# Kernel tuning notes

Hardware: AMD Instinct MI355X
Metric: run time of the kernel (lower is better)

## Reference

```python
import jax, jax.numpy as jnp
import numpy as np

N_NODES = 50000
N_EDGES = 800000
N_GRAPHS = 8
BN_EPS = 1e-5


def setup_inputs() -> dict:
    key = jax.random.key(0)
    ks = iter(jax.random.split(key, 40))
    d = {}
    d["x"] = jax.random.normal(next(ks), (N_NODES, 3), dtype=jnp.float32)
    d["edge_index"] = jax.random.randint(next(ks), (2, N_EDGES), 0, N_NODES, dtype=jnp.int32)
    d["batch"] = jnp.sort(jax.random.randint(next(ks), (N_NODES,), 0, N_GRAPHS, dtype=jnp.int32))
    conv_in = [3, 64, 128]  # dense concat widths feeding each GCN layer
    for i, cin in enumerate(conv_in):
        d[f"W{i}"] = jax.random.normal(next(ks), (cin, 64), dtype=jnp.float32) * (1.0 / np.sqrt(cin))
        d[f"b{i}"] = jax.random.normal(next(ks), (64,), dtype=jnp.float32) * 0.05
        d[f"g{i}"] = jax.random.uniform(next(ks), (64,), dtype=jnp.float32) + 0.5
        d[f"beta{i}"] = jax.random.normal(next(ks), (64,), dtype=jnp.float32) * 0.05
        d[f"rm{i}"] = jax.random.normal(next(ks), (64,), dtype=jnp.float32) * 0.05
        d[f"rv{i}"] = jax.random.uniform(next(ks), (64,), dtype=jnp.float32) + 0.5
    def lin(k, i, o):
        return (jax.random.normal(k, (i, o), dtype=jnp.float32) * (1.0 / np.sqrt(i)),)
    d["enc_w0"], = lin(next(ks), 256, 128); d["enc_b0"] = jax.random.normal(next(ks), (128,), jnp.float32) * 0.05
    d["enc_w1"], = lin(next(ks), 128, 64); d["enc_b1"] = jax.random.normal(next(ks), (64,), jnp.float32) * 0.05
    d["dec_w0"], = lin(next(ks), 64, 32); d["dec_b0"] = jax.random.normal(next(ks), (32,), jnp.float32) * 0.05
    d["dec_w1"], = lin(next(ks), 32, 1); d["dec_b1"] = jax.random.normal(next(ks), (1,), jnp.float32) * 0.05
    return d


def reference(x, edge_index, batch,
              W0, b0, g0, beta0, rm0, rv0,
              W1, b1, g1, beta1, rm1, rv1,
              W2, b2, g2, beta2, rm2, rv2,
              enc_w0, enc_b0, enc_w1, enc_b1,
              dec_w0, dec_b0, dec_w1, dec_b1):
    N = x.shape[0]
    loops = jnp.arange(N, dtype=edge_index.dtype)
    src = jnp.concatenate([edge_index[0], loops])  # GCNConv adds self loops
    dst = jnp.concatenate([edge_index[1], loops])
    deg = jax.ops.segment_sum(jnp.ones_like(src, dtype=x.dtype), dst, num_segments=N)
    dinv = jnp.where(deg > 0, jax.lax.rsqrt(deg), 0.0)
    coef = (dinv[src] * dinv[dst])[:, None]  # symmetric normalization per edge

    def conv_bn_relu(h, W, b, g, beta, rm, rv):
        hw = h @ W                                    # [N, 64]
        out = jax.ops.segment_sum(hw[src] * coef, dst, num_segments=N) + b
        out = (out - rm) * (g * jax.lax.rsqrt(rv + BN_EPS)) + beta  # BN eval mode
        return jax.nn.relu(out)

    params = [(W0, b0, g0, beta0, rm0, rv0),
              (W1, b1, g1, beta1, rm1, rv1),
              (W2, b2, g2, beta2, rm2, rv2)]
    prev = []
    h = x
    for p in params:  # dense connectivity: concat all previous concat-outputs
        h = conv_bn_relu(h, *p)
        h = jnp.concatenate(prev + [h], axis=1)
        prev.append(h)

    e = jax.nn.relu(jax.nn.relu(h @ enc_w0 + enc_b0) @ enc_w1 + enc_b1)  # [N, 64]
    counts = jax.ops.segment_sum(jnp.ones((N,), x.dtype), batch, num_segments=N_GRAPHS)
    gfeat = jax.ops.segment_sum(e, batch, num_segments=N_GRAPHS) / jnp.maximum(counts, 1.0)[:, None]
    out = jax.nn.relu(gfeat @ dec_w0 + dec_b0) @ dec_w1 + dec_b1  # [G, 1]
    return out[:, 0]  # torch.squeeze(output, 1) since num_classes == 1
```

## Files before the change

kernel.cpp:

```cpp
#include <hip/hip_runtime.h>
#include <hip/hip_fp16.h>

#define NN 50000
#define NE 800000
#define NG 8
#define BN_EPS 1e-5f
#define NBLK ((NN + 255) / 256)
#define POOL_BLOCKS 512
#define NPART 8
#define HLD 192

typedef __attribute__((ext_vector_type(8))) short bf16x8;
typedef __attribute__((ext_vector_type(4))) float f32x4;

static __device__ __forceinline__ unsigned short f2bf(float f) {
    unsigned int u = __float_as_uint(f);
    unsigned int r = (u + 0x7FFFu + ((u >> 16) & 1u)) >> 16;
    return (unsigned short)r;
}
static __device__ __forceinline__ float bf2f(unsigned short h) {
    return __uint_as_float((unsigned int)h << 16);
}


__global__ __launch_bounds__(256) void count_deg(const int* __restrict__ dst,
                                                 int* __restrict__ degi) {
    int e = blockIdx.x * 256 + threadIdx.x;
    if (e < NE) atomicAdd(&degi[dst[e]], 1);
}

__global__ __launch_bounds__(256) void compute_dinv_xs(const int* __restrict__ degi,
                                                       const float* __restrict__ x,
                                                       float* __restrict__ dinv,
                                                       float* __restrict__ xs) {
    int i = blockIdx.x * 256 + threadIdx.x;
    if (i < NN) {
        float di = rsqrtf((float)(degi[i] + 1));
        dinv[i] = di;
        xs[i * 3 + 0] = x[i * 3 + 0] * di;
        xs[i * 3 + 1] = x[i * 3 + 1] * di;
        xs[i * 3 + 2] = x[i * 3 + 2] * di;
    }
}

__global__ __launch_bounds__(256) void scan_partial(const int* __restrict__ degi,
                                                    int* __restrict__ rowptr,
                                                    int* __restrict__ bsum) {
    __shared__ int sh[256];
    const int tid = threadIdx.x;
    const int i = blockIdx.x * 256 + tid;
    int v = (i < NN) ? degi[i] : 0;
    sh[tid] = v;
    __syncthreads();
#pragma unroll
    for (int off = 1; off < 256; off <<= 1) {
        int t = (tid >= off) ? sh[tid - off] : 0;
        __syncthreads();
        sh[tid] += t;
        __syncthreads();
    }
    if (i < NN) rowptr[i] = sh[tid] - v;
    if (tid == 255) bsum[blockIdx.x] = sh[255];
}

__global__ __launch_bounds__(256) void scan_bsums(int* __restrict__ bsum) {
    __shared__ int sh[256];
    const int tid = threadIdx.x;
    int v = (tid < NBLK) ? bsum[tid] : 0;
    sh[tid] = v;
    __syncthreads();
#pragma unroll
    for (int off = 1; off < 256; off <<= 1) {
        int t = (tid >= off) ? sh[tid - off] : 0;
        __syncthreads();
        sh[tid] += t;
        __syncthreads();
    }
    if (tid < NBLK) bsum[tid] = sh[tid] - v;
}

__global__ __launch_bounds__(256) void scan_finalize(const int* __restrict__ bsum,
                                                     int* __restrict__ rowptr,
                                                     int* __restrict__ cursor) {
    const int i = blockIdx.x * 256 + threadIdx.x;
    if (i < NN) {
        int r = rowptr[i] + bsum[blockIdx.x];
        rowptr[i] = r;
        cursor[i] = r;
    }
    if (i == 0) rowptr[NN] = NE;
}

__global__ __launch_bounds__(256) void fill_csr(const int* __restrict__ src,
                                                const int* __restrict__ dst,
                                                int* __restrict__ cursor,
                                                unsigned short* __restrict__ esrc16) {
    int e = blockIdx.x * 256 + threadIdx.x;
    if (e < NE) {
        int s = src[e], d = dst[e];
        int p = atomicAdd(&cursor[d], 1);
        esrc16[p] = (unsigned short)s;
    }
}


__global__ __launch_bounds__(256) void pack_w(const float* __restrict__ W, int K, int NOUT,
                                              unsigned short* __restrict__ ph,
                                              unsigned short* __restrict__ pl) {
    int idx = blockIdx.x * 256 + threadIdx.x;
    if (idx >= K * NOUT) return;
    int j = idx & 7;
    int lane = (idx >> 3) & 63;
    int rest = idx >> 9;
    int NF = NOUT >> 4;
    int f = rest % NF, ks = rest / NF;
    int k = ks * 32 + (lane >> 4) * 8 + j;
    int col = f * 16 + (lane & 15);
    float v = W[k * NOUT + col];
    unsigned short hi = f2bf(v);
    ph[idx] = hi;
    pl[idx] = f2bf(v - bf2f(hi));
}

__global__ __launch_bounds__(256) void pack_we0(const float* __restrict__ W,
                                                unsigned short* __restrict__ ph,
                                                unsigned short* __restrict__ pl) {
    const int K = 192, NOUT = 128;
    int idx = blockIdx.x * 256 + threadIdx.x;
    if (idx >= K * NOUT) return;
    int j = idx & 7;
    int lane = (idx >> 3) & 63;
    int rest = idx >> 9;
    int NF = NOUT >> 4;
    int f = rest % NF, ks = rest / NF;
    int k = ks * 32 + (lane >> 4) * 8 + j;
    int col = f * 16 + (lane & 15);
    float v = (k < 64) ? (W[k * NOUT + col] + W[(k + 64) * NOUT + col])
                       : W[(k + 64) * NOUT + col];
    unsigned short hi = f2bf(v);
    ph[idx] = hi;
    pl[idx] = f2bf(v - bf2f(hi));
}


template<int K, int NF, int MODE>
__global__ __launch_bounds__(256) void mfma_gemm(
        const unsigned short* __restrict__ Ahi,
        const unsigned short* __restrict__ Alo, int lda,
        const unsigned short* __restrict__ Bph,
        const unsigned short* __restrict__ Bpl,
        const float* __restrict__ bias,
        const float* __restrict__ dinv,
        float* __restrict__ outF,
        __half* __restrict__ outH,
        unsigned short* __restrict__ outHi,
        unsigned short* __restrict__ outLo, int ldo) {
    const int wave = threadIdx.x >> 6;
    const int lane = threadIdx.x & 63;
    const int rbase = blockIdx.x * 64 + wave * 16;
    int arow = rbase + (lane & 15);
    if (arow >= NN) arow = NN - 1;
    const int kbase = (lane >> 4) * 8;

    f32x4 acc[NF];
#pragma unroll
    for (int f = 0; f < NF; f++) acc[f] = (f32x4){0.f, 0.f, 0.f, 0.f};

    const unsigned short* pa_hi = Ahi + (size_t)arow * lda + kbase;
    const unsigned short* pa_lo = Alo + (size_t)arow * lda + kbase;
    const unsigned short* pb_hi = Bph + lane * 8;
    const unsigned short* pb_lo = Bpl + lane * 8;

#pragma unroll
    for (int ks = 0; ks < K / 32; ks++) {
        bf16x8 ah = *reinterpret_cast<const bf16x8*>(pa_hi + ks * 32);
        bf16x8 al = *reinterpret_cast<const bf16x8*>(pa_lo + ks * 32);
#pragma unroll
        for (int f = 0; f < NF; f++) {
            bf16x8 bh = *reinterpret_cast<const bf16x8*>(pb_hi + (size_t)((ks * NF + f) * 64) * 8);
            bf16x8 bl = *reinterpret_cast<const bf16x8*>(pb_lo + (size_t)((ks * NF + f) * 64) * 8);
            acc[f] = __builtin_amdgcn_mfma_f32_16x16x32_bf16(ah, bh, acc[f], 0, 0, 0);
            acc[f] = __builtin_amdgcn_mfma_f32_16x16x32_bf16(ah, bl, acc[f], 0, 0, 0);
            acc[f] = __builtin_amdgcn_mfma_f32_16x16x32_bf16(al, bh, acc[f], 0, 0, 0);
        }
    }

    const int drow0 = rbase + (lane >> 4) * 4;
    const int dcol = lane & 15;
#pragma unroll
    for (int f = 0; f < NF; f++) {
#pragma unroll
        for (int r = 0; r < 4; r++) {
            int row = drow0 + r;
            if (row < NN) {
                int col = f * 16 + dcol;
                float v = acc[f][r];
                if (MODE == 0) {
                    outH[(size_t)row * 64 + col] = __float2half(v * dinv[row]);
                } else {
                    v = fmaxf(v + bias[col], 0.0f);
                    if (MODE == 1) {
                        unsigned short hi = f2bf(v);
                        outHi[(size_t)row * ldo + col] = hi;
                        outLo[(size_t)row * ldo + col] = f2bf(v - bf2f(hi));
                    } else {
                        outF[(size_t)row * ldo + col] = v;
                    }
                }
            }
        }
    }
}


__global__ __launch_bounds__(256) void agg_x3(
        const float* __restrict__ xs,
        const int* __restrict__ rowptr,
        const unsigned short* __restrict__ esrc16,
        const float* __restrict__ dinv,
        float* __restrict__ ax) {
    const int i = blockIdx.x * 256 + threadIdx.x;
    if (i >= NN) return;
    float a0 = xs[i * 3 + 0];
    float a1 = xs[i * 3 + 1];
    float a2 = xs[i * 3 + 2];
    const int beg = rowptr[i], end = rowptr[i + 1];
    int e = beg;
    for (; e + 3 < end; e += 4) {
        int s0 = esrc16[e], s1 = esrc16[e + 1], s2 = esrc16[e + 2], s3 = esrc16[e + 3];
        a0 += xs[s0 * 3 + 0] + xs[s1 * 3 + 0] + xs[s2 * 3 + 0] + xs[s3 * 3 + 0];
        a1 += xs[s0 * 3 + 1] + xs[s1 * 3 + 1] + xs[s2 * 3 + 1] + xs[s3 * 3 + 1];
        a2 += xs[s0 * 3 + 2] + xs[s1 * 3 + 2] + xs[s2 * 3 + 2] + xs[s3 * 3 + 2];
    }
    for (; e < end; e++) {
        int s = esrc16[e];
        a0 += xs[s * 3 + 0];
        a1 += xs[s * 3 + 1];
        a2 += xs[s * 3 + 2];
    }
    const float di = dinv[i];
    ax[i * 3 + 0] = a0 * di;
    ax[i * 3 + 1] = a1 * di;
    ax[i * 3 + 2] = a2 * di;
}


__global__ __launch_bounds__(256) void l0_bn_relu(
        const float* __restrict__ ax, const float* __restrict__ W0,
        const float* __restrict__ b, const float* __restrict__ g,
        const float* __restrict__ beta, const float* __restrict__ rm,
        const float* __restrict__ rv,
        unsigned short* __restrict__ Hhi, unsigned short* __restrict__ Hlo) {
    const int t = blockIdx.x * 256 + threadIdx.x;
    const int row = t >> 6;
    const int ch = t & 63;
    if (row >= NN) return;
    float a0 = ax[row * 3 + 0], a1 = ax[row * 3 + 1], a2 = ax[row * 3 + 2];
    float v = a0 * W0[0 * 64 + ch] + a1 * W0[1 * 64 + ch] + a2 * W0[2 * 64 + ch] + b[ch];
    float sc = g[ch] * rsqrtf(rv[ch] + BN_EPS);
    v = (v - rm[ch]) * sc + beta[ch];
    v = fmaxf(v, 0.0f);
    unsigned short hi = f2bf(v);
    Hhi[(size_t)row * HLD + ch] = hi;
    Hlo[(size_t)row * HLD + ch] = f2bf(v - bf2f(hi));
}


__global__ __launch_bounds__(256) void gather_bn_relu(
        const __half2* __restrict__ tab2,
        const int* __restrict__ rowptr,
        const unsigned short* __restrict__ esrc16,
        const float* __restrict__ dinv,
        const float* __restrict__ b, const float* __restrict__ g,
        const float* __restrict__ beta, const float* __restrict__ rm,
        const float* __restrict__ rv,
        unsigned short* __restrict__ Hhi, unsigned short* __restrict__ Hlo, int cbase) {
    const int wid = (blockIdx.x * 256 + threadIdx.x) >> 6;
    const int lane = threadIdx.x & 63;
    const int c2 = lane & 31;
    const int grp = lane >> 5;
    if (wid >= NN) return;
    const int beg = rowptr[wid], end = rowptr[wid + 1];
    float a0 = 0.0f, a1 = 0.0f;
    int e = beg + grp;
    for (; e + 6 < end; e += 8) {
        int s0 = esrc16[e], s1 = esrc16[e + 2], s2 = esrc16[e + 4], s3 = esrc16[e + 6];
        float2 f0 = __half22float2(tab2[(size_t)s0 * 32 + c2]);
        float2 f1 = __half22float2(tab2[(size_t)s1 * 32 + c2]);
        float2 f2 = __half22float2(tab2[(size_t)s2 * 32 + c2]);
        float2 f3 = __half22float2(tab2[(size_t)s3 * 32 + c2]);
        a0 += (f0.x + f1.x) + (f2.x + f3.x);
        a1 += (f0.y + f1.y) + (f2.y + f3.y);
    }
    for (; e < end; e += 2) {
        float2 f = __half22float2(tab2[(size_t)esrc16[e] * 32 + c2]);
        a0 += f.x;
        a1 += f.y;
    }
    a0 += __shfl_xor(a0, 32, 64);
    a1 += __shfl_xor(a1, 32, 64);
    float2 fs = __half22float2(tab2[(size_t)wid * 32 + c2]);
    a0 += fs.x;
    a1 += fs.y;
    const float di = dinv[wid];
    a0 *= di;
    a1 *= di;
    const int ch0 = 2 * c2, ch1 = 2 * c2 + 1;
    float v0 = (a0 + b[ch0] - rm[ch0]) * (g[ch0] * rsqrtf(rv[ch0] + BN_EPS)) + beta[ch0];
    float v1 = (a1 + b[ch1] - rm[ch1]) * (g[ch1] * rsqrtf(rv[ch1] + BN_EPS)) + beta[ch1];
    v0 = fmaxf(v0, 0.0f);
    v1 = fmaxf(v1, 0.0f);
    if (grp == 0) {
        unsigned short h0 = f2bf(v0), h1 = f2bf(v1);
        unsigned short l0 = f2bf(v0 - bf2f(h0)), l1 = f2bf(v1 - bf2f(h1));
        size_t o = (size_t)wid * HLD + cbase + ch0;
        *reinterpret_cast<unsigned int*>(&Hhi[o]) = (unsigned int)h0 | ((unsigned int)h1 << 16);
        *reinterpret_cast<unsigned int*>(&Hlo[o]) = (unsigned int)l0 | ((unsigned int)l1 << 16);
    }
}


__global__ __launch_bounds__(256) void pool_kernel(
        const float* __restrict__ e, const int* __restrict__ batch,
        float* __restrict__ gfeat_part, float* __restrict__ counts_part) {
    __shared__ float sh[4][NG][64];
    __shared__ float shc[4][NG];
    const int tid = threadIdx.x;
    const int ch = tid & 63;
    const int rg = tid >> 6;
    float acc[NG];
    float cnt[NG];
#pragma unroll
    for (int g = 0; g < NG; g++) { acc[g] = 0.0f; cnt[g] = 0.0f; }
    for (int i = blockIdx.x * 4 + rg; i < NN; i += POOL_BLOCKS * 4) {
        int b = batch[i];
        float v = e[i * 64 + ch];
#pragma unroll
        for (int g = 0; g < NG; g++) {
            acc[g] += (b == g) ? v : 0.0f;
            cnt[g] += (b == g) ? 1.0f : 0.0f;
        }
    }
#pragma unroll
    for (int g = 0; g < NG; g++) sh[rg][g][ch] = acc[g];
    if (ch == 0) {
#pragma unroll
        for (int g = 0; g < NG; g++) shc[rg][g] = cnt[g];
    }
    __syncthreads();
    const int p = blockIdx.x & (NPART - 1);
    if (rg == 0) {
#pragma unroll
        for (int g = 0; g < NG; g++) {
            float s = sh[0][g][ch] + sh[1][g][ch] + sh[2][g][ch] + sh[3][g][ch];
            atomicAdd(&gfeat_part[(p * NG + g) * 64 + ch], s);
        }
    }
    if (tid < NG) {
        float s = shc[0][tid] + shc[1][tid] + shc[2][tid] + shc[3][tid];
        atomicAdd(&counts_part[p * NG + tid], s);
    }
}


__global__ __launch_bounds__(256) void dec_kernel(
        const float* __restrict__ gfeat_part, const float* __restrict__ counts_part,
        const float* __restrict__ w0, const float* __restrict__ b0,
        const float* __restrict__ w1, const float* __restrict__ b1,
        float* __restrict__ out) {
    __shared__ float mg[NG][64];
    __shared__ float mc[NG];
    __shared__ float t1[NG][32];
    const int tid = threadIdx.x;
    for (int idx = tid; idx < NG * 64; idx += 256) {
        float s = 0.0f;
#pragma unroll
        for (int p = 0; p < NPART; p++) s += gfeat_part[p * NG * 64 + idx];
        mg[idx >> 6][idx & 63] = s;
    }
    if (tid < NG) {
        float s = 0.0f;
#pragma unroll
        for (int p = 0; p < NPART; p++) s += counts_part[p * NG + tid];
        mc[tid] = s;
    }
    __syncthreads();
    const int g = tid >> 5, c = tid & 31;
    float inv = 1.0f / fmaxf(mc[g], 1.0f);
    float acc = b0[c];
    for (int k = 0; k < 64; k++)
        acc = fmaf(mg[g][k] * inv, w0[k * 32 + c], acc);
    t1[g][c] = fmaxf(acc, 0.0f);
    __syncthreads();
    if (tid < NG) {
        float o = b1[0];
        for (int c2 = 0; c2 < 32; c2++) o = fmaf(t1[tid][c2], w1[c2], o);
        out[tid] = o;
    }
}


extern "C" void kernel_launch(void* const* d_in, const int* in_sizes, int n_in,
                              void* d_out, int out_size, void* d_ws, size_t ws_size,
                              hipStream_t stream) {
    const float* x      = (const float*)d_in[0];
    const int*   ei     = (const int*)d_in[1];
    const int*   batch  = (const int*)d_in[2];
    const float* W0     = (const float*)d_in[3];
    const float* b0     = (const float*)d_in[4];
    const float* g0     = (const float*)d_in[5];
    const float* beta0  = (const float*)d_in[6];
    const float* rm0    = (const float*)d_in[7];
    const float* rv0    = (const float*)d_in[8];
    const float* W1     = (const float*)d_in[9];
    const float* b1     = (const float*)d_in[10];
    const float* g1     = (const float*)d_in[11];
    const float* beta1  = (const float*)d_in[12];
    const float* rm1    = (const float*)d_in[13];
    const float* rv1    = (const float*)d_in[14];
    const float* W2     = (const float*)d_in[15];
    const float* b2     = (const float*)d_in[16];
    const float* g2     = (const float*)d_in[17];
    const float* beta2  = (const float*)d_in[18];
    const float* rm2    = (const float*)d_in[19];
    const float* rv2    = (const float*)d_in[20];
    const float* enc_w0 = (const float*)d_in[21];
    const float* enc_b0 = (const float*)d_in[22];
    const float* enc_w1 = (const float*)d_in[23];
    const float* enc_b1 = (const float*)d_in[24];
    const float* dec_w0 = (const float*)d_in[25];
    const float* dec_b0 = (const float*)d_in[26];
    const float* dec_w1 = (const float*)d_in[27];
    const float* dec_b1 = (const float*)d_in[28];

    const int* esrc = ei;
    const int* edst = ei + NE;

    char* wsb = (char*)d_ws;
    unsigned short* Hhi = (unsigned short*)wsb;
    unsigned short* Hlo = Hhi + (size_t)NN * HLD;
    char* U = (char*)(Hlo + (size_t)NN * HLD);
    unsigned short* Thi = (unsigned short*)U;
    unsigned short* Tlo = Thi + (size_t)NN * 128;
    int*   degi   = (int*)U;
    int*   rowptr = degi + NN;
    int*   cursor = rowptr + NN + 1;
    unsigned short* esrc16 = (unsigned short*)(cursor + NN);
    float* hws    = (float*)(U + (size_t)NN * 128 * 2 * sizeof(unsigned short));
    __half* tabh  = (__half*)hws;
    float* dinv   = hws + (size_t)NN * 64;
    float* xs     = dinv + NN;
    float* ax     = xs + (size_t)NN * 3;
    float* gfeat_part  = ax + (size_t)NN * 3;
    float* counts_part = gfeat_part + NPART * NG * 64;
    int*   bsum   = (int*)(counts_part + NPART * NG);
    unsigned short* wp = (unsigned short*)(bsum + NBLK);
    unsigned short* Wp1h = wp;              unsigned short* Wp1l = Wp1h + 64 * 64;
    unsigned short* Wp2h = Wp1l + 64 * 64;  unsigned short* Wp2l = Wp2h + 128 * 64;
    unsigned short* We0h = Wp2l + 128 * 64; unsigned short* We0l = We0h + 192 * 128;
    unsigned short* We1h = We0l + 192 * 128;unsigned short* We1l = We1h + 128 * 64;

    hipMemsetAsync(gfeat_part, 0, (NPART * NG * 64 + NPART * NG) * sizeof(float), stream);
    hipMemsetAsync(degi, 0, NN * sizeof(int), stream);

    count_deg<<<(NE + 255) / 256, 256, 0, stream>>>(edst, degi);
    compute_dinv_xs<<<NBLK, 256, 0, stream>>>(degi, x, dinv, xs);
    scan_partial<<<NBLK, 256, 0, stream>>>(degi, rowptr, bsum);
    scan_bsums<<<1, 256, 0, stream>>>(bsum);
    scan_finalize<<<NBLK, 256, 0, stream>>>(bsum, rowptr, cursor);
    fill_csr<<<(NE + 255) / 256, 256, 0, stream>>>(esrc, edst, cursor, esrc16);

    pack_w<<<(64 * 64 + 255) / 256, 256, 0, stream>>>(W1, 64, 64, Wp1h, Wp1l);
    pack_w<<<(128 * 64 + 255) / 256, 256, 0, stream>>>(W2, 128, 64, Wp2h, Wp2l);
    pack_we0<<<(192 * 128 + 255) / 256, 256, 0, stream>>>(enc_w0, We0h, We0l);
    pack_w<<<(128 * 64 + 255) / 256, 256, 0, stream>>>(enc_w1, 128, 64, We1h, We1l);

    const int GRID_MFMA = (NN + 63) / 64;
    const int GRID_64   = (NN * 64 + 255) / 256;

    agg_x3<<<NBLK, 256, 0, stream>>>(xs, rowptr, esrc16, dinv, ax);
    l0_bn_relu<<<GRID_64, 256, 0, stream>>>(ax, W0, b0, g0, beta0, rm0, rv0, Hhi, Hlo);

    mfma_gemm<64, 4, 0><<<GRID_MFMA, 256, 0, stream>>>(Hhi, Hlo, HLD, Wp1h, Wp1l,
                                                       nullptr, dinv, nullptr, tabh, nullptr, nullptr, 0);
    gather_bn_relu<<<GRID_64, 256, 0, stream>>>((const __half2*)tabh, rowptr, esrc16, dinv,
                                                b1, g1, beta1, rm1, rv1, Hhi, Hlo, 64);

    mfma_gemm<128, 4, 0><<<GRID_MFMA, 256, 0, stream>>>(Hhi, Hlo, HLD, Wp2h, Wp2l,
                                                        nullptr, dinv, nullptr, tabh, nullptr, nullptr, 0);
    gather_bn_relu<<<GRID_64, 256, 0, stream>>>((const __half2*)tabh, rowptr, esrc16, dinv,
                                                b2, g2, beta2, rm2, rv2, Hhi, Hlo, 128);

    mfma_gemm<192, 8, 1><<<GRID_MFMA, 256, 0, stream>>>(Hhi, Hlo, HLD, We0h, We0l,
                                                        enc_b0, nullptr, nullptr, nullptr, Thi, Tlo, 128);
    mfma_gemm<128, 4, 2><<<GRID_MFMA, 256, 0, stream>>>(Thi, Tlo, 128, We1h, We1l,
                                                        enc_b1, nullptr, hws, nullptr, nullptr, nullptr, 64);

    pool_kernel<<<POOL_BLOCKS, 256, 0, stream>>>(hws, batch, gfeat_part, counts_part);
    dec_kernel<<<1, 256, 0, stream>>>(gfeat_part, counts_part, dec_w0, dec_b0, dec_w1, dec_b1, (float*)d_out);
}
```

Baseline: 260.5 us.

## Fuse encoder GEMMs with mean pooling and merge small setup kernels

Fuses the two encoder GEMMs and the graph pooling into one kernel. The first GEMM's output stays in LDS and is re-split into bf16 hi/lo pairs for the second GEMM, and results are pooled through shared-memory atomics. This removes the global round trips for the 128-wide intermediate and the 64-wide encoder output, plus the separate pool kernel. The dinv/xs computation is folded into the scan kernel, the four weight-packing launches become one, and per-graph counts come from a binary search over the sorted batch array. The cost is more shared-memory atomics, LDS pressure from a 34KB buffer, and one extra block-wide sync.

```diff
diff --git a/kernel.cpp b/kernel.cpp
--- a/kernel.cpp
+++ b/kernel.cpp
@@ -6,7 +6,6 @@
 #define NG 8
 #define BN_EPS 1e-5f
 #define NBLK ((NN + 255) / 256)
-#define POOL_BLOCKS 512
 #define NPART 8
 #define HLD 192
 
@@ -29,27 +28,23 @@
     if (e < NE) atomicAdd(&degi[dst[e]], 1);
 }
 
-__global__ __launch_bounds__(256) void compute_dinv_xs(const int* __restrict__ degi,
-                                                       const float* __restrict__ x,
-                                                       float* __restrict__ dinv,
-                                                       float* __restrict__ xs) {
-    int i = blockIdx.x * 256 + threadIdx.x;
+__global__ __launch_bounds__(256) void scan_partial(const int* __restrict__ degi,
+                                                    const float* __restrict__ x,
+                                                    int* __restrict__ rowptr,
+                                                    int* __restrict__ bsum,
+                                                    float* __restrict__ dinv,
+                                                    float* __restrict__ xs) {
+    __shared__ int sh[256];
+    const int tid = threadIdx.x;
+    const int i = blockIdx.x * 256 + tid;
+    int v = (i < NN) ? degi[i] : 0;
     if (i < NN) {
-        float di = rsqrtf((float)(degi[i] + 1));
+        float di = rsqrtf((float)(v + 1));
         dinv[i] = di;
         xs[i * 3 + 0] = x[i * 3 + 0] * di;
         xs[i * 3 + 1] = x[i * 3 + 1] * di;
         xs[i * 3 + 2] = x[i * 3 + 2] * di;
     }
-}
-
-__global__ __launch_bounds__(256) void scan_partial(const int* __restrict__ degi,
-                                                    int* __restrict__ rowptr,
-                                                    int* __restrict__ bsum) {
-    __shared__ int sh[256];
-    const int tid = threadIdx.x;
-    const int i = blockIdx.x * 256 + tid;
-    int v = (i < NN) ? degi[i] : 0;
     sh[tid] = v;
     __syncthreads();
 #pragma unroll
@@ -104,57 +99,59 @@
 }
 
 
-__global__ __launch_bounds__(256) void pack_w(const float* __restrict__ W, int K, int NOUT,
-                                              unsigned short* __restrict__ ph,
-                                              unsigned short* __restrict__ pl) {
-    int idx = blockIdx.x * 256 + threadIdx.x;
-    if (idx >= K * NOUT) return;
-    int j = idx & 7;
-    int lane = (idx >> 3) & 63;
-    int rest = idx >> 9;
+static __device__ __forceinline__ void pack_one(const float* W, int NOUT, int li,
+                                                float v_override, bool use_override,
+                                                unsigned short* ph, unsigned short* pl) {
+    int j = li & 7;
+    int lane = (li >> 3) & 63;
+    int rest = li >> 9;
     int NF = NOUT >> 4;
     int f = rest % NF, ks = rest / NF;
     int k = ks * 32 + (lane >> 4) * 8 + j;
     int col = f * 16 + (lane & 15);
-    float v = W[k * NOUT + col];
+    float v = use_override ? v_override : W[k * NOUT + col];
     unsigned short hi = f2bf(v);
-    ph[idx] = hi;
-    pl[idx] = f2bf(v - bf2f(hi));
-}
-
-__global__ __launch_bounds__(256) void pack_we0(const float* __restrict__ W,
-                                                unsigned short* __restrict__ ph,
-                                                unsigned short* __restrict__ pl) {
-    const int K = 192, NOUT = 128;
+    ph[li] = hi;
+    pl[li] = f2bf(v - bf2f(hi));
+}
+
+__global__ __launch_bounds__(256) void pack_all(
+        const float* __restrict__ W1, const float* __restrict__ W2,
+        const float* __restrict__ We0, const float* __restrict__ We1,
+        unsigned short* __restrict__ Wp1h, unsigned short* __restrict__ Wp1l,
+        unsigned short* __restrict__ Wp2h, unsigned short* __restrict__ Wp2l,
+        unsigned short* __restrict__ We0h, unsigned short* __restrict__ We0l,
+        unsigned short* __restrict__ We1h, unsigned short* __restrict__ We1l) {
     int idx = blockIdx.x * 256 + threadIdx.x;
-    if (idx >= K * NOUT) return;
-    int j = idx & 7;
-    int lane = (idx >> 3) & 63;
-    int rest = idx >> 9;
-    int NF = NOUT >> 4;
-    int f = rest % NF, ks = rest / NF;
-    int k = ks * 32 + (lane >> 4) * 8 + j;
-    int col = f * 16 + (lane & 15);
-    float v = (k < 64) ? (W[k * NOUT + col] + W[(k + 64) * NOUT + col])
-                       : W[(k + 64) * NOUT + col];
-    unsigned short hi = f2bf(v);
-    ph[idx] = hi;
-    pl[idx] = f2bf(v - bf2f(hi));
-}
-
-
-template<int K, int NF, int MODE>
-__global__ __launch_bounds__(256) void mfma_gemm(
+    if (idx < 4096) {
+        pack_one(W1, 64, idx, 0.f, false, Wp1h, Wp1l);
+    } else if (idx < 12288) {
+        pack_one(W2, 64, idx - 4096, 0.f, false, Wp2h, Wp2l);
+    } else if (idx < 36864) {
+        int li = idx - 12288;
+        int j = li & 7;
+        int lane = (li >> 3) & 63;
+        int rest = li >> 9;
+        int f = rest % 8, ks = rest / 8;
+        int k = ks * 32 + (lane >> 4) * 8 + j;
+        int col = f * 16 + (lane & 15);
+        float v = (k < 64) ? (We0[k * 128 + col] + We0[(k + 64) * 128 + col])
+                           : We0[(k + 64) * 128 + col];
+        pack_one(nullptr, 128, li, v, true, We0h, We0l);
+    } else if (idx < 45056) {
+        pack_one(We1, 64, idx - 36864, 0.f, false, We1h, We1l);
+    }
+}
+
+
+template<int K>
+__global__ __launch_bounds__(256) void mfma_tab(
         const unsigned short* __restrict__ Ahi,
         const unsigned short* __restrict__ Alo, int lda,
         const unsigned short* __restrict__ Bph,
         const unsigned short* __restrict__ Bpl,
-        const float* __restrict__ bias,
         const float* __restrict__ dinv,
-        float* __restrict__ outF,
-        __half* __restrict__ outH,
-        unsigned short* __restrict__ outHi,
-        unsigned short* __restrict__ outLo, int ldo) {
+        __half* __restrict__ outH) {
     const int wave = threadIdx.x >> 6;
     const int lane = threadIdx.x & 63;
     const int rbase = blockIdx.x * 64 + wave * 16;
@@ -162,9 +159,9 @@
     if (arow >= NN) arow = NN - 1;
     const int kbase = (lane >> 4) * 8;
 
-    f32x4 acc[NF];
-#pragma unroll
-    for (int f = 0; f < NF; f++) acc[f] = (f32x4){0.f, 0.f, 0.f, 0.f};
+    f32x4 acc[4];
+#pragma unroll
+    for (int f = 0; f < 4; f++) acc[f] = (f32x4){0.f, 0.f, 0.f, 0.f};
 
     const unsigned short* pa_hi = Ahi + (size_t)arow * lda + kbase;
     const unsigned short* pa_lo = Alo + (size_t)arow * lda + kbase;
@@ -176,9 +173,9 @@
         bf16x8 ah = *reinterpret_cast<const bf16x8*>(pa_hi + ks * 32);
         bf16x8 al = *reinterpret_cast<const bf16x8*>(pa_lo + ks * 32);
 #pragma unroll
-        for (int f = 0; f < NF; f++) {
-            bf16x8 bh = *reinterpret_cast<const bf16x8*>(pb_hi + (size_t)((ks * NF + f) * 64) * 8);
-            bf16x8 bl = *reinterpret_cast<const bf16x8*>(pb_lo + (size_t)((ks * NF + f) * 64) * 8);
+        for (int f = 0; f < 4; f++) {
+            bf16x8 bh = *reinterpret_cast<const bf16x8*>(pb_hi + (size_t)((ks * 4 + f) * 64) * 8);
+            bf16x8 bl = *reinterpret_cast<const bf16x8*>(pb_lo + (size_t)((ks * 4 + f) * 64) * 8);
             acc[f] = __builtin_amdgcn_mfma_f32_16x16x32_bf16(ah, bh, acc[f], 0, 0, 0);
             acc[f] = __builtin_amdgcn_mfma_f32_16x16x32_bf16(ah, bl, acc[f], 0, 0, 0);
             acc[f] = __builtin_amdgcn_mfma_f32_16x16x32_bf16(al, bh, acc[f], 0, 0, 0);
@@ -188,28 +185,113 @@
     const int drow0 = rbase + (lane >> 4) * 4;
     const int dcol = lane & 15;
 #pragma unroll
-    for (int f = 0; f < NF; f++) {
+    for (int f = 0; f < 4; f++) {
 #pragma unroll
         for (int r = 0; r < 4; r++) {
             int row = drow0 + r;
-            if (row < NN) {
+            if (row < NN)
+                outH[(size_t)row * 64 + f * 16 + dcol] = __float2half(acc[f][r] * dinv[row]);
+        }
+    }
+}
+
+
+__global__ __launch_bounds__(256) void enc_fused(
+        const unsigned short* __restrict__ Hhi,
+        const unsigned short* __restrict__ Hlo,
+        const unsigned short* __restrict__ We0h, const unsigned short* __restrict__ We0l,
+        const float* __restrict__ b0,
+        const unsigned short* __restrict__ We1h, const unsigned short* __restrict__ We1l,
+        const float* __restrict__ b1,
+        const int* __restrict__ batch,
+        float* __restrict__ gfeat_part) {
+    __shared__ float ldsT[4][16][133];
+    __shared__ float pool[NG][64];
+    const int tid = threadIdx.x;
+    const int wave = tid >> 6;
+    const int lane = tid & 63;
+    const int rbase = blockIdx.x * 64 + wave * 16;
+
+    for (int i = tid; i < NG * 64; i += 256) ((float*)pool)[i] = 0.0f;
+
+    int arow = rbase + (lane & 15);
+    if (arow >= NN) arow = NN - 1;
+    const int kbase = (lane >> 4) * 8;
+    f32x4 acc[8];
+#pragma unroll
+    for (int f = 0; f < 8; f++) acc[f] = (f32x4){0.f, 0.f, 0.f, 0.f};
+
+    const unsigned short* pa_hi = Hhi + (size_t)arow * HLD + kbase;
+    const unsigned short* pa_lo = Hlo + (size_t)arow * HLD + kbase;
+#pragma unroll
+    for (int ks = 0; ks < 6; ks++) {
+        bf16x8 ah = *reinterpret_cast<const bf16x8*>(pa_hi + ks * 32);
+        bf16x8 al = *reinterpret_cast<const bf16x8*>(pa_lo + ks * 32);
+#pragma unroll
+        for (int f = 0; f < 8; f++) {
+            bf16x8 bh = *reinterpret_cast<const bf16x8*>(We0h + (size_t)(((ks * 8 + f) * 64 + lane)) * 8);
+            bf16x8 bl = *reinterpret_cast<const bf16x8*>(We0l + (size_t)(((ks * 8 + f) * 64 + lane)) * 8);
+            acc[f] = __builtin_amdgcn_mfma_f32_16x16x32_bf16(ah, bh, acc[f], 0, 0, 0);
+            acc[f] = __builtin_amdgcn_mfma_f32_16x16x32_bf16(ah, bl, acc[f], 0, 0, 0);
+            acc[f] = __builtin_amdgcn_mfma_f32_16x16x32_bf16(al, bh, acc[f], 0, 0, 0);
+        }
+    }
+
+    const int lrow0 = (lane >> 4) * 4;
+    const int dcol = lane & 15;
+#pragma unroll
+    for (int f = 0; f < 8; f++) {
+#pragma unroll
+        for (int r = 0; r < 4; r++) {
+            float v = fmaxf(acc[f][r] + b0[f * 16 + dcol], 0.0f);
+            ldsT[wave][lrow0 + r][f * 16 + dcol] = v;
+        }
+    }
+    __syncthreads();
+
+    f32x4 acc2[4];
+#pragma unroll
+    for (int f = 0; f < 4; f++) acc2[f] = (f32x4){0.f, 0.f, 0.f, 0.f};
+
+    const int trow = lane & 15;
+#pragma unroll
+    for (int ks = 0; ks < 4; ks++) {
+        bf16x8 ah, al;
+#pragma unroll
+        for (int j = 0; j < 8; j++) {
+            float tv = ldsT[wave][trow][ks * 32 + (lane >> 4) * 8 + j];
+            unsigned short hi = f2bf(tv);
+            ah[j] = (short)hi;
+            al[j] = (short)f2bf(tv - bf2f(hi));
+        }
+#pragma unroll
+        for (int f = 0; f < 4; f++) {
+            bf16x8 bh = *reinterpret_cast<const bf16x8*>(We1h + (size_t)(((ks * 4 + f) * 64 + lane)) * 8);
+            bf16x8 bl = *reinterpret_cast<const bf16x8*>(We1l + (size_t)(((ks * 4 + f) * 64 + lane)) * 8);
+            acc2[f] = __builtin_amdgcn_mfma_f32_16x16x32_bf16(ah, bh, acc2[f], 0, 0, 0);
+            acc2[f] = __builtin_amdgcn_mfma_f32_16x16x32_bf16(ah, bl, acc2[f], 0, 0, 0);
+            acc2[f] = __builtin_amdgcn_mfma_f32_16x16x32_bf16(al, bh, acc2[f], 0, 0, 0);
+        }
+    }
+
+#pragma unroll
+    for (int r = 0; r < 4; r++) {
+        int row = rbase + lrow0 + r;
+        if (row < NN) {
+            int g = batch[row];
+#pragma unroll
+            for (int f = 0; f < 4; f++) {
                 int col = f * 16 + dcol;
-                float v = acc[f][r];
-                if (MODE == 0) {
-                    outH[(size_t)row * 64 + col] = __float2half(v * dinv[row]);
-                } else {
-                    v = fmaxf(v + bias[col], 0.0f);
-                    if (MODE == 1) {
-                        unsigned short hi = f2bf(v);
-                        outHi[(size_t)row * ldo + col] = hi;
-                        outLo[(size_t)row * ldo + col] = f2bf(v - bf2f(hi));
-                    } else {
-                        outF[(size_t)row * ldo + col] = v;
-                    }
-                }
+                float v = fmaxf(acc2[f][r] + b1[col], 0.0f);
+                atomicAdd(&pool[g][col], v);
             }
         }
     }
+    __syncthreads();
+
+    const int p = blockIdx.x & (NPART - 1);
+    for (int i = tid; i < NG * 64; i += 256)
+        atomicAdd(&gfeat_part[p * NG * 64 + i], ((float*)pool)[i]);
 }
 
 
@@ -320,51 +402,8 @@
 }
 
 
-__global__ __launch_bounds__(256) void pool_kernel(
-        const float* __restrict__ e, const int* __restrict__ batch,
-        float* __restrict__ gfeat_part, float* __restrict__ counts_part) {
-    __shared__ float sh[4][NG][64];
-    __shared__ float shc[4][NG];
-    const int tid = threadIdx.x;
-    const int ch = tid & 63;
-    const int rg = tid >> 6;
-    float acc[NG];
-    float cnt[NG];
-#pragma unroll
-    for (int g = 0; g < NG; g++) { acc[g] = 0.0f; cnt[g] = 0.0f; }
-    for (int i = blockIdx.x * 4 + rg; i < NN; i += POOL_BLOCKS * 4) {
-        int b = batch[i];
-        float v = e[i * 64 + ch];
-#pragma unroll
-        for (int g = 0; g < NG; g++) {
-            acc[g] += (b == g) ? v : 0.0f;
-            cnt[g] += (b == g) ? 1.0f : 0.0f;
-        }
-    }
-#pragma unroll
-    for (int g = 0; g < NG; g++) sh[rg][g][ch] = acc[g];
-    if (ch == 0) {
-#pragma unroll
-        for (int g = 0; g < NG; g++) shc[rg][g] = cnt[g];
-    }
-    __syncthreads();
-    const int p = blockIdx.x & (NPART - 1);
-    if (rg == 0) {
-#pragma unroll
-        for (int g = 0; g < NG; g++) {
-            float s = sh[0][g][ch] + sh[1][g][ch] + sh[2][g][ch] + sh[3][g][ch];
-            atomicAdd(&gfeat_part[(p * NG + g) * 64 + ch], s);
-        }
-    }
-    if (tid < NG) {
-        float s = shc[0][tid] + shc[1][tid] + shc[2][tid] + shc[3][tid];
-        atomicAdd(&counts_part[p * NG + tid], s);
-    }
-}
-
-
 __global__ __launch_bounds__(256) void dec_kernel(
-        const float* __restrict__ gfeat_part, const float* __restrict__ counts_part,
+        const float* __restrict__ gfeat_part, const int* __restrict__ batch,
         const float* __restrict__ w0, const float* __restrict__ b0,
         const float* __restrict__ w1, const float* __restrict__ b1,
         float* __restrict__ out) {
@@ -379,10 +418,12 @@
         mg[idx >> 6][idx & 63] = s;
     }
     if (tid < NG) {
-        float s = 0.0f;
-#pragma unroll
-        for (int p = 0; p < NPART; p++) s += counts_part[p * NG + tid];
-        mc[tid] = s;
+        int lo = 0, hi = NN;
+        while (lo < hi) { int m = (lo + hi) >> 1; if (batch[m] < tid) lo = m + 1; else hi = m; }
+        int s0 = lo;
+        lo = 0; hi = NN;
+        while (lo < hi) { int m = (lo + hi) >> 1; if (batch[m] < tid + 1) lo = m + 1; else hi = m; }
+        mc[tid] = (float)(lo - s0);
     }
     __syncthreads();
     const int g = tid >> 5, c = tid & 31;
@@ -439,41 +480,34 @@
     char* wsb = (char*)d_ws;
     unsigned short* Hhi = (unsigned short*)wsb;
     unsigned short* Hlo = Hhi + (size_t)NN * HLD;
-    char* U = (char*)(Hlo + (size_t)NN * HLD);
-    unsigned short* Thi = (unsigned short*)U;
-    unsigned short* Tlo = Thi + (size_t)NN * 128;
-    int*   degi   = (int*)U;
+    int*   degi   = (int*)(Hlo + (size_t)NN * HLD);
     int*   rowptr = degi + NN;
     int*   cursor = rowptr + NN + 1;
     unsigned short* esrc16 = (unsigned short*)(cursor + NN);
-    float* hws    = (float*)(U + (size_t)NN * 128 * 2 * sizeof(unsigned short));
-    __half* tabh  = (__half*)hws;
-    float* dinv   = hws + (size_t)NN * 64;
+    __half* tabh  = (__half*)(esrc16 + NE);
+    float* dinv   = (float*)(tabh + (size_t)NN * 64);
     float* xs     = dinv + NN;
     float* ax     = xs + (size_t)NN * 3;
-    float* gfeat_part  = ax + (size_t)NN * 3;
-    float* counts_part = gfeat_part + NPART * NG * 64;
-    int*   bsum   = (int*)(counts_part + NPART * NG);
+    float* gfeat_part = ax + (size_t)NN * 3;
+    int*   bsum   = (int*)(gfeat_part + NPART * NG * 64);
     unsigned short* wp = (unsigned short*)(bsum + NBLK);
     unsigned short* Wp1h = wp;              unsigned short* Wp1l = Wp1h + 64 * 64;
     unsigned short* Wp2h = Wp1l + 64 * 64;  unsigned short* Wp2l = Wp2h + 128 * 64;
     unsigned short* We0h = Wp2l + 128 * 64; unsigned short* We0l = We0h + 192 * 128;
     unsigned short* We1h = We0l + 192 * 128;unsigned short* We1l = We1h + 128 * 64;
 
-    hipMemsetAsync(gfeat_part, 0, (NPART * NG * 64 + NPART * NG) * sizeof(float), stream);
+    hipMemsetAsync(gfeat_part, 0, NPART * NG * 64 * sizeof(float), stream);
     hipMemsetAsync(degi, 0, NN * sizeof(int), stream);
 
     count_deg<<<(NE + 255) / 256, 256, 0, stream>>>(edst, degi);
-    compute_dinv_xs<<<NBLK, 256, 0, stream>>>(degi, x, dinv, xs);
-    scan_partial<<<NBLK, 256, 0, stream>>>(degi, rowptr, bsum);
+    scan_partial<<<NBLK, 256, 0, stream>>>(degi, x, rowptr, bsum, dinv, xs);
     scan_bsums<<<1, 256, 0, stream>>>(bsum);
     scan_finalize<<<NBLK, 256, 0, stream>>>(bsum, rowptr, cursor);
     fill_csr<<<(NE + 255) / 256, 256, 0, stream>>>(esrc, edst, cursor, esrc16);
 
-    pack_w<<<(64 * 64 + 255) / 256, 256, 0, stream>>>(W1, 64, 64, Wp1h, Wp1l);
-    pack_w<<<(128 * 64 + 255) / 256, 256, 0, stream>>>(W2, 128, 64, Wp2h, Wp2l);
-    pack_we0<<<(192 * 128 + 255) / 256, 256, 0, stream>>>(enc_w0, We0h, We0l);
-    pack_w<<<(128 * 64 + 255) / 256, 256, 0, stream>>>(enc_w1, 128, 64, We1h, We1l);
+    pack_all<<<(45056 + 255) / 256, 256, 0, stream>>>(W1, W2, enc_w0, enc_w1,
+                                                      Wp1h, Wp1l, Wp2h, Wp2l,
+                                                      We0h, We0l, We1h, We1l);
 
     const int GRID_MFMA = (NN + 63) / 64;
     const int GRID_64   = (NN * 64 + 255) / 256;
@@ -481,21 +515,16 @@
     agg_x3<<<NBLK, 256, 0, stream>>>(xs, rowptr, esrc16, dinv, ax);
     l0_bn_relu<<<GRID_64, 256, 0, stream>>>(ax, W0, b0, g0, beta0, rm0, rv0, Hhi, Hlo);
 
-    mfma_gemm<64, 4, 0><<<GRID_MFMA, 256, 0, stream>>>(Hhi, Hlo, HLD, Wp1h, Wp1l,
-                                                       nullptr, dinv, nullptr, tabh, nullptr, nullptr, 0);
+    mfma_tab<64><<<GRID_MFMA, 256, 0, stream>>>(Hhi, Hlo, HLD, Wp1h, Wp1l, dinv, tabh);
     gather_bn_relu<<<GRID_64, 256, 0, stream>>>((const __half2*)tabh, rowptr, esrc16, dinv,
                                                 b1, g1, beta1, rm1, rv1, Hhi, Hlo, 64);
 
-    mfma_gemm<128, 4, 0><<<GRID_MFMA, 256, 0, stream>>>(Hhi, Hlo, HLD, Wp2h, Wp2l,
-                                                        nullptr, dinv, nullptr, tabh, nullptr, nullptr, 0);
+    mfma_tab<128><<<GRID_MFMA, 256, 0, stream>>>(Hhi, Hlo, HLD, Wp2h, Wp2l, dinv, tabh);
     gather_bn_relu<<<GRID_64, 256, 0, stream>>>((const __half2*)tabh, rowptr, esrc16, dinv,
                                                 b2, g2, beta2, rm2, rv2, Hhi, Hlo, 128);
 
-    mfma_gemm<192, 8, 1><<<GRID_MFMA, 256, 0, stream>>>(Hhi, Hlo, HLD, We0h, We0l,
-                                                        enc_b0, nullptr, nullptr, nullptr, Thi, Tlo, 128);
-    mfma_gemm<128, 4, 2><<<GRID_MFMA, 256, 0, stream>>>(Thi, Tlo, 128, We1h, We1l,
-                                                        enc_b1, nullptr, hws, nullptr, nullptr, nullptr, 64);
-
-    pool_kernel<<<POOL_BLOCKS, 256, 0, stream>>>(hws, batch, gfeat_part, counts_part);
-    dec_kernel<<<1, 256, 0, stream>>>(gfeat_part, counts_part, dec_w0, dec_b0, dec_w1, dec_b1, (float*)d_out);
-}
+    enc_fused<<<GRID_MFMA, 256, 0, stream>>>(Hhi, Hlo, We0h, We0l, enc_b0,
+                                             We1h, We1l, enc_b1, batch, gfeat_part);
+
+    dec_kernel<<<1, 256, 0, stream>>>(gfeat_part, batch, dec_w0, dec_b0, dec_w1, dec_b1, (float*)d_out);
+}
```

After: 261.4 us. About the same (+0.4%).
